# Kernel optimization log

Measured on AMD Instinct MI355X. Metric: run time of the kernel, lower is better.

The kernel has to match this reference:

```python
import jax, jax.numpy as jnp
import numpy as np

T = 64      # simulation_length
B = 128     # batch
D = 2048    # flattened input dim / axons per core
N = 2048    # neurons per core
L = 4       # number of cores (chain, latency = index)
OUT = 1024  # number of output_sources


def setup_inputs() -> dict:
    key = jax.random.key(0)
    k0, k1, k2, k3 = jax.random.split(key, 4)
    x = jax.random.uniform(k0, (B, D), dtype=jnp.float32)          # rate-coded input in [0,1)
    # core_params[l] = core_matrix.transpose() -> shape [N, A]; scaled for sane membrane dynamics
    W = jax.random.normal(k1, (L, N, D), dtype=jnp.float32) * 0.05
    thresholds = jnp.ones((L,), dtype=jnp.float32)
    # axon_sources: per-core irregular gather indices into previous core's neurons (input for l=0)
    axon_idx = jax.random.randint(k2, (L, D), 0, D, dtype=jnp.int32)
    out_idx = jax.random.randint(k3, (OUT,), 0, N, dtype=jnp.int32)
    return dict(x=x, W=W, thresholds=thresholds, axon_idx=axon_idx,
                out_idx=out_idx, simulation_length=T)


def _ideal_spike_scan(avg, thr, T):
    """Per-cycle: m += avg; spike = (m > thr); m[m > thr] -= thr.  avg: [B, N]."""
    def step(m, _):
        m = m + avg
        s = (m > thr).astype(m.dtype)
        return m - thr * s, s
    _, spikes = jax.lax.scan(step, jnp.zeros_like(avg), None, length=T)
    return spikes  # [T, B, N]


def reference(x, W, thresholds, axon_idx, out_idx, simulation_length):
    T = simulation_length
    L = W.shape[0]
    # generate_input_spike_train: x replicated across all cycles -> cache[-1]
    prev = jnp.broadcast_to(x, (T,) + x.shape)  # [T, B, D]
    for l in range(L):
        # get_signal_tensor: gather axon source signals for every cycle
        gathered = prev[:, :, axon_idx[l]]                    # [T, B, A]
        # per-cycle matmul: torch.matmul(core_params, sig.T).T == sig @ W[l].T
        val = jnp.einsum('tba,na->tbn', gathered, W[l])       # [T, B, N]
        avg = val.mean(axis=0)                                # avg_values [B, N]
        # ideal membrane integrate + threshold-reset recurrence -> out spike train
        prev = _ideal_spike_scan(avg, thresholds[l], T)       # [T, B, N]
    # output_signals: sum of output-source spikes over all cycles
    return prev[:, :, out_idx].sum(axis=0)                    # [B, OUT]
```

## Files before the change

### kernel.cpp

```cpp
#include <hip/hip_runtime.h>

#define BB   128
#define DD   2048
#define NN   2048
#define LL   4
#define OUTN 1024
#define JBQ  32
#define NDIG 5

#define NWDIG 12288
#define NG0   1024
#define NCSR  4

typedef double double4v __attribute__((ext_vector_type(4)));
typedef int    int4v    __attribute__((ext_vector_type(4)));
typedef char   char4v   __attribute__((ext_vector_type(4)));

__global__ __launch_bounds__(256) void prep_kernel(
    const float* __restrict__ W1,
    const float* __restrict__ x,
    const int*   __restrict__ axon,
    const int*   __restrict__ oidx,
    signed char* __restrict__ Wd,
    float*       __restrict__ At,
    int*         __restrict__ off,
    int*         __restrict__ lst)
{
    __shared__ int hist[2048];
    __shared__ int part[256];

    const int t  = threadIdx.x;
    const int bk = blockIdx.x;
    const size_t DP = (size_t)NN * DD;

    if (bk < NWDIG) {
        size_t i  = (size_t)bk * 256 + t;
        int    l  = (int)(i / (DP / 4));
        size_t e4 = i - (size_t)l * (DP / 4);
        int n = (int)(e4 >> 9);
        int k = (int)(e4 & 511) * 4;
        float4 w = *(const float4*)(W1 + (size_t)l * DP + (size_t)n * DD + k);
        const float wv[4] = {w.x, w.y, w.z, w.w};
        unsigned long long V[4];
        #pragma unroll
        for (int e = 0; e < 4; ++e)
            V[e] = (unsigned long long)(__double2ll_rn((double)wv[e] * 0x1p33)
                                        + (1LL << 34));
        signed char* base = Wd + (size_t)l * 5 * DP
                          + (size_t)(n >> 5) * 65536 + (size_t)(k >> 6) * 2048
                          + (n & 31) * 64 + (k & 63);
        #pragma unroll
        for (int j = 0; j < NDIG; ++j) {
            char4v p = { (char)((V[0] >> (7 * j)) & 127),
                         (char)((V[1] >> (7 * j)) & 127),
                         (char)((V[2] >> (7 * j)) & 127),
                         (char)((V[3] >> (7 * j)) & 127) };
            *(char4v*)(base + (size_t)j * DP) = p;
        }
        return;
    }
    if (bk < NWDIG + NG0) {
        int i = (bk - NWDIG) * 256 + t;
        int k = i >> 7;
        int b = i & 127;
        At[i] = x[b * DD + axon[k]];
        return;
    }
    {
        const int m   = bk - (NWDIG + NG0);
        const int* ip = (m < 3) ? (axon + (size_t)(m + 1) * DD) : oidx;
        const int cnt = (m < 3) ? DD : OUTN;
        int* offG = off + m * 2052;
        int* lstG = lst + m * 2048;

        for (int i = t; i < 2048; i += 256) hist[i] = 0;
        __syncthreads();
        for (int e = t; e < cnt; e += 256) atomicAdd(&hist[ip[e]], 1);
        __syncthreads();

        const int b0 = t * 8;
        int s = 0;
        #pragma unroll
        for (int i = 0; i < 8; ++i) s += hist[b0 + i];
        part[t] = s;
        __syncthreads();
        for (int d = 1; d < 256; d <<= 1) {
            int v = (t >= d) ? part[t - d] : 0;
            __syncthreads();
            part[t] += v;
            __syncthreads();
        }
        int base = part[t] - s;
        #pragma unroll
        for (int i = 0; i < 8; ++i) {
            int h = hist[b0 + i];
            offG[b0 + i] = base;
            hist[b0 + i] = base;
            base += h;
        }
        if (t == 255) offG[2048] = base;
        __syncthreads();
        for (int e = t; e < cnt; e += 256) {
            int n = ip[e];
            int pos = atomicAdd(&hist[n], 1);
            lstG[pos] = e;
        }
    }
}

__global__ __launch_bounds__(256, 2) void layer_kernel(
    const float* __restrict__ src,
    const int*   __restrict__ idx,
    int sR, int sB,
    const float* __restrict__ Wl,
    const float* __restrict__ thresholds, int l,
    const int*   __restrict__ Tptr,
    float* __restrict__ dst,
    const int* __restrict__ goff, const int* __restrict__ glst,
    signed char* __restrict__ g8n,
    const int* __restrict__ ooff, const int* __restrict__ olst,
    float* __restrict__ outp,
    int isLast)
{
    __shared__ double red[4 * 64 * 8];

    const int t    = threadIdx.x;
    const int wq   = t >> 6;
    const int lane = t & 63;
    const int q    = lane >> 4;
    const int c    = lane & 15;

    const int g     = blockIdx.x;
    const int btile = (g >> 3) & 7;
    const int nsup  = (g & 7) | ((g >> 6) << 3);
    const int n0    = nsup * 32;
    const int bcol  = btile * 16 + c;
    const size_t bo = (size_t)bcol * sB;

    double4v pr = {0., 0., 0., 0.}, pcv = {0., 0., 0., 0.};
    pr  = __builtin_amdgcn_mfma_f64_16x16x4f64(0.25 * (double)c, 1.0, pr, 0, 0, 0);
    pcv = __builtin_amdgcn_mfma_f64_16x16x4f64(0.25, (double)c, pcv, 0, 0, 0);
    int rowD[4], colD[4];
    #pragma unroll
    for (int r = 0; r < 4; ++r) {
        rowD[r] = (int)(pr[r] + 0.25);
        colD[r] = (int)(pcv[r] + 0.25);
    }

    double4v acc0[4] = {{0.,0.,0.,0.},{0.,0.,0.,0.},{0.,0.,0.,0.},{0.,0.,0.,0.}};
    double4v acc1[4] = {{0.,0.,0.,0.},{0.,0.,0.,0.},{0.,0.,0.,0.},{0.,0.,0.,0.}};

    const int    kbase = wq * (DD / 4);
    const float* wb0   = Wl + (size_t)(n0 + c) * DD + kbase + 4 * q;
    const float* wb1   = wb0 + (size_t)16 * DD;
    const int*   ibase = idx ? (idx + kbase + 4 * q) : nullptr;

    float4 wv0[4], wv1[4];
    float4 sv[4];
    int4   iv[4];

    #pragma unroll
    for (int p = 0; p < 4; ++p) {
        wv0[p] = *(const float4*)(wb0 + 16 * p);
        wv1[p] = *(const float4*)(wb1 + 16 * p);
    }
    #pragma unroll
    for (int p = 0; p < 4; ++p) {
        int r0, r1, r2, r3;
        if (ibase) {
            int4 iv0 = *(const int4*)(ibase + 16 * p);
            r0 = iv0.x; r1 = iv0.y; r2 = iv0.z; r3 = iv0.w;
        } else {
            int kb = kbase + 16 * p + 4 * q;
            r0 = kb; r1 = kb + 1; r2 = kb + 2; r3 = kb + 3;
        }
        sv[p].x = src[(size_t)r0 * sR + bo];
        sv[p].y = src[(size_t)r1 * sR + bo];
        sv[p].z = src[(size_t)r2 * sR + bo];
        sv[p].w = src[(size_t)r3 * sR + bo];
    }
    if (ibase) {
        #pragma unroll
        for (int p = 0; p < 4; ++p) iv[p] = *(const int4*)(ibase + 16 * (4 + p));
    }

    for (int u = 0; u < JBQ / 4; ++u) {
        #pragma unroll
        for (int gg = 0; gg < 4; ++gg) {
            float4 w0 = wv0[gg];
            float4 w1 = wv1[gg];
            float4 s  = sv[gg];

            int jn = 4 * u + 4 + gg; if (jn > JBQ - 1) jn = JBQ - 1;
            wv0[gg] = *(const float4*)(wb0 + 16 * jn);
            wv1[gg] = *(const float4*)(wb1 + 16 * jn);

            int r0, r1, r2, r3;
            if (ibase) {
                int4 ivv = iv[gg];
                r0 = ivv.x; r1 = ivv.y; r2 = ivv.z; r3 = ivv.w;
            } else {
                int kb = kbase + 16 * jn + 4 * q;
                r0 = kb; r1 = kb + 1; r2 = kb + 2; r3 = kb + 3;
            }
            sv[gg].x = src[(size_t)r0 * sR + bo];
            sv[gg].y = src[(size_t)r1 * sR + bo];
            sv[gg].z = src[(size_t)r2 * sR + bo];
            sv[gg].w = src[(size_t)r3 * sR + bo];

            if (ibase) {
                int jm = 4 * u + 8 + gg; if (jm > JBQ - 1) jm = JBQ - 1;
                iv[gg] = *(const int4*)(ibase + 16 * jm);
            }

            acc0[0] = __builtin_amdgcn_mfma_f64_16x16x4f64((double)w0.x, (double)s.x, acc0[0], 0, 0, 0);
            acc1[0] = __builtin_amdgcn_mfma_f64_16x16x4f64((double)w1.x, (double)s.x, acc1[0], 0, 0, 0);
            acc0[1] = __builtin_amdgcn_mfma_f64_16x16x4f64((double)w0.y, (double)s.y, acc0[1], 0, 0, 0);
            acc1[1] = __builtin_amdgcn_mfma_f64_16x16x4f64((double)w1.y, (double)s.y, acc1[1], 0, 0, 0);
            acc0[2] = __builtin_amdgcn_mfma_f64_16x16x4f64((double)w0.z, (double)s.z, acc0[2], 0, 0, 0);
            acc1[2] = __builtin_amdgcn_mfma_f64_16x16x4f64((double)w1.z, (double)s.z, acc1[2], 0, 0, 0);
            acc0[3] = __builtin_amdgcn_mfma_f64_16x16x4f64((double)w0.w, (double)s.w, acc0[3], 0, 0, 0);
            acc1[3] = __builtin_amdgcn_mfma_f64_16x16x4f64((double)w1.w, (double)s.w, acc1[3], 0, 0, 0);
        }
    }

    double4v a0 = (acc0[0] + acc0[1]) + (acc0[2] + acc0[3]);
    double4v a1 = (acc1[0] + acc1[1]) + (acc1[2] + acc1[3]);

    {
        double* my = red + ((size_t)wq * 64 + lane) * 8;
        #pragma unroll
        for (int r = 0; r < 4; ++r) { my[r] = a0[r]; my[4 + r] = a1[r]; }
    }
    __syncthreads();
    if (wq < 2) {
        const int off = wq * 4;
        double a[4];
        #pragma unroll
        for (int r = 0; r < 4; ++r) {
            a[r] =  red[((size_t)0 * 64 + lane) * 8 + off + r];
            a[r] += red[((size_t)1 * 64 + lane) * 8 + off + r];
            a[r] += red[((size_t)2 * 64 + lane) * 8 + off + r];
            a[r] += red[((size_t)3 * 64 + lane) * 8 + off + r];
        }

        const double th = (double)thresholds[l];
        const int T = *Tptr;
        const float sc = isLast ? 1.0f : (1.0f / (float)T);
        double m0 = 0., m1 = 0., m2 = 0., m3 = 0.;
        int c0 = 0, c1 = 0, c2 = 0, c3 = 0;
        for (int tt = 0; tt < T; ++tt) {
            m0 += a[0]; if (m0 > th) { c0++; m0 -= th; }
            m1 += a[1]; if (m1 > th) { c1++; m1 -= th; }
            m2 += a[2]; if (m2 > th) { c2++; m2 -= th; }
            m3 += a[3]; if (m3 > th) { c3++; m3 -= th; }
        }
        int cnt[4] = {c0, c1, c2, c3};
        #pragma unroll
        for (int r = 0; r < 4; ++r) {
            int n = n0 + 16 * wq + rowD[r];
            int b = btile * 16 + colD[r];
            if (dst)  dst[(size_t)n * BB + b] = (float)cnt[r] * sc;
            if (goff) {
                for (int j = goff[n]; j < goff[n + 1]; ++j) {
                    int k = glst[j];
                    g8n[(size_t)(k >> 6) * 8192 + b * 64 + (k & 63)] =
                        (signed char)cnt[r];
                }
            }
            if (ooff) {
                for (int j = ooff[n]; j < ooff[n + 1]; ++j)
                    outp[(size_t)b * OUTN + olst[j]] = (float)cnt[r];
            }
        }
    }
}

__global__ __launch_bounds__(256, 2) void layer_i8_kernel(
    const signed char* __restrict__ B8,
    const signed char* __restrict__ Wd5,
    const float* __restrict__ thresholds, int l,
    const int*   __restrict__ Tptr,
    const int* __restrict__ goff, const int* __restrict__ glst,
    signed char* __restrict__ g8n,
    const int* __restrict__ ooff, const int* __restrict__ olst,
    float* __restrict__ outp,
    int isLast)
{
    __shared__ double red[4 * 64 * 8];

    const int t    = threadIdx.x;
    const int wq   = t >> 6;
    const int lane = t & 63;
    const int q    = lane >> 4;
    const int c    = lane & 15;

    const int g     = blockIdx.x;
    const int btile = (g >> 3) & 7;
    const int nsup  = (g & 7) | ((g >> 6) << 3);
    const int n0    = nsup * 32;
    const int bcol  = btile * 16 + c;

    int rowD[4], colD[4];
    {
        const int cb  = c * 0x01010101;
        const int hot = (q == 0) ? 1 : 0;
        int4v aLab = {cb, cb, cb, cb};
        int4v oneh = {hot, 0, 0, 0};
        int4v dR = {0, 0, 0, 0}, dC = {0, 0, 0, 0};
        dR = __builtin_amdgcn_mfma_i32_16x16x64_i8(aLab, oneh, dR, 0, 0, 0);
        dC = __builtin_amdgcn_mfma_i32_16x16x64_i8(oneh, aLab, dC, 0, 0, 0);
        #pragma unroll
        for (int r = 0; r < 4; ++r) { rowD[r] = dR[r]; colD[r] = dC[r]; }
    }

    int4v acc0[NDIG], acc1[NDIG], accS = (int4v)0;
    #pragma unroll
    for (int j = 0; j < NDIG; ++j) { acc0[j] = (int4v)0; acc1[j] = (int4v)0; }

    const size_t DP = (size_t)NN * DD;
    const signed char* ab = Wd5 + (size_t)nsup * 65536 + c * 64 + q * 16;
    const signed char* bb = B8 + bcol * 64 + q * 16;

    const int4v ones = {0x01010101, 0x01010101, 0x01010101, 0x01010101};
    const int ck0 = wq * 8;

    int4v A0[NDIG], A1[NDIG], Bv;
    int4v N0[NDIG], N1[NDIG], Nb;

    {
        const signed char* ap = ab + (size_t)ck0 * 2048;
        #pragma unroll
        for (int j = 0; j < NDIG; ++j) {
            A0[j] = *(const int4v*)(ap + (size_t)j * DP);
            A1[j] = *(const int4v*)(ap + (size_t)j * DP + 1024);
        }
        Bv = *(const int4v*)(bb + (size_t)ck0 * 8192);
    }

    #pragma unroll 1
    for (int u = 0; u < 3; ++u) {
        {
            const signed char* ap = ab + (size_t)(ck0 + 2 * u + 1) * 2048;
            #pragma unroll
            for (int j = 0; j < NDIG; ++j) {
                N0[j] = *(const int4v*)(ap + (size_t)j * DP);
                N1[j] = *(const int4v*)(ap + (size_t)j * DP + 1024);
            }
            Nb = *(const int4v*)(bb + (size_t)(ck0 + 2 * u + 1) * 8192);
        }
        #pragma unroll
        for (int j = 0; j < NDIG; ++j) {
            acc0[j] = __builtin_amdgcn_mfma_i32_16x16x64_i8(A0[j], Bv, acc0[j], 0, 0, 0);
            acc1[j] = __builtin_amdgcn_mfma_i32_16x16x64_i8(A1[j], Bv, acc1[j], 0, 0, 0);
        }
        accS = __builtin_amdgcn_mfma_i32_16x16x64_i8(ones, Bv, accS, 0, 0, 0);
        {
            const signed char* ap = ab + (size_t)(ck0 + 2 * u + 2) * 2048;
            #pragma unroll
            for (int j = 0; j < NDIG; ++j) {
                A0[j] = *(const int4v*)(ap + (size_t)j * DP);
                A1[j] = *(const int4v*)(ap + (size_t)j * DP + 1024);
            }
            Bv = *(const int4v*)(bb + (size_t)(ck0 + 2 * u + 2) * 8192);
        }
        #pragma unroll
        for (int j = 0; j < NDIG; ++j) {
            acc0[j] = __builtin_amdgcn_mfma_i32_16x16x64_i8(N0[j], Nb, acc0[j], 0, 0, 0);
            acc1[j] = __builtin_amdgcn_mfma_i32_16x16x64_i8(N1[j], Nb, acc1[j], 0, 0, 0);
        }
        accS = __builtin_amdgcn_mfma_i32_16x16x64_i8(ones, Nb, accS, 0, 0, 0);
    }
    {
        const signed char* ap = ab + (size_t)(ck0 + 7) * 2048;
        #pragma unroll
        for (int j = 0; j < NDIG; ++j) {
            N0[j] = *(const int4v*)(ap + (size_t)j * DP);
            N1[j] = *(const int4v*)(ap + (size_t)j * DP + 1024);
        }
        Nb = *(const int4v*)(bb + (size_t)(ck0 + 7) * 8192);
    }
    #pragma unroll
    for (int j = 0; j < NDIG; ++j) {
        acc0[j] = __builtin_amdgcn_mfma_i32_16x16x64_i8(A0[j], Bv, acc0[j], 0, 0, 0);
        acc1[j] = __builtin_amdgcn_mfma_i32_16x16x64_i8(A1[j], Bv, acc1[j], 0, 0, 0);
    }
    accS = __builtin_amdgcn_mfma_i32_16x16x64_i8(ones, Bv, accS, 0, 0, 0);
    #pragma unroll
    for (int j = 0; j < NDIG; ++j) {
        acc0[j] = __builtin_amdgcn_mfma_i32_16x16x64_i8(N0[j], Nb, acc0[j], 0, 0, 0);
        acc1[j] = __builtin_amdgcn_mfma_i32_16x16x64_i8(N1[j], Nb, acc1[j], 0, 0, 0);
    }
    accS = __builtin_amdgcn_mfma_i32_16x16x64_i8(ones, Nb, accS, 0, 0, 0);

    const double S0 = 0x1p-33, S1 = 0x1p-26, S2 = 0x1p-19,
                 S3 = 0x1p-12, S4 = 0x1p-5;
    {
        double* my = red + ((size_t)wq * 64 + lane) * 8;
        #pragma unroll
        for (int r = 0; r < 4; ++r) {
            double corr = 2.0 * (double)accS[r];
            my[r]     = S0 * (double)acc0[0][r] + S1 * (double)acc0[1][r]
                      + S2 * (double)acc0[2][r] + S3 * (double)acc0[3][r]
                      + S4 * (double)acc0[4][r] - corr;
            my[4 + r] = S0 * (double)acc1[0][r] + S1 * (double)acc1[1][r]
                      + S2 * (double)acc1[2][r] + S3 * (double)acc1[3][r]
                      + S4 * (double)acc1[4][r] - corr;
        }
    }
    __syncthreads();
    if (wq < 2) {
        const int off = wq * 4;
        double a[4];
        #pragma unroll
        for (int r = 0; r < 4; ++r) {
            a[r] =  red[((size_t)0 * 64 + lane) * 8 + off + r];
            a[r] += red[((size_t)1 * 64 + lane) * 8 + off + r];
            a[r] += red[((size_t)2 * 64 + lane) * 8 + off + r];
            a[r] += red[((size_t)3 * 64 + lane) * 8 + off + r];
        }

        const double th = (double)thresholds[l];
        const int T = *Tptr;
        const double invT = 1.0 / (double)T;
        double m0 = 0., m1 = 0., m2 = 0., m3 = 0.;
        int c0 = 0, c1 = 0, c2 = 0, c3 = 0;
        const double v0 = a[0] * invT, v1 = a[1] * invT,
                     v2 = a[2] * invT, v3 = a[3] * invT;
        for (int tt = 0; tt < T; ++tt) {
            m0 += v0; if (m0 > th) { c0++; m0 -= th; }
            m1 += v1; if (m1 > th) { c1++; m1 -= th; }
            m2 += v2; if (m2 > th) { c2++; m2 -= th; }
            m3 += v3; if (m3 > th) { c3++; m3 -= th; }
        }
        int cnt[4] = {c0, c1, c2, c3};
        #pragma unroll
        for (int r = 0; r < 4; ++r) {
            int n = n0 + 16 * wq + rowD[r];
            int b = btile * 16 + colD[r];
            if (goff) {
                for (int j = goff[n]; j < goff[n + 1]; ++j) {
                    int k = glst[j];
                    g8n[(size_t)(k >> 6) * 8192 + b * 64 + (k & 63)] =
                        (signed char)cnt[r];
                }
            }
            if (ooff) {
                for (int j = ooff[n]; j < ooff[n + 1]; ++j)
                    outp[(size_t)b * OUTN + olst[j]] = (float)cnt[r];
            }
        }
    }
}

__global__ __launch_bounds__(256) void out_kernel(
    const float* __restrict__ cntT, const int* __restrict__ out_idx,
    float* __restrict__ out)
{
    int i = blockIdx.x * 256 + threadIdx.x;
    int b = i >> 10;
    int o = i & 1023;
    out[i] = cntT[(size_t)out_idx[o] * BB + b];
}

extern "C" void kernel_launch(void* const* d_in, const int* in_sizes, int n_in,
                              void* d_out, int out_size, void* d_ws, size_t ws_size,
                              hipStream_t stream)
{
    const float* x    = (const float*)d_in[0];
    const float* W    = (const float*)d_in[1];
    const float* thr  = (const float*)d_in[2];
    const int*   axon = (const int*)d_in[3];
    const int*   oidx = (const int*)d_in[4];
    const int*   Tptr = (const int*)d_in[5];
    float* out = (float*)d_out;

    const size_t DP = (size_t)NN * DD;
    char* ws = (char*)d_ws;
    float* At   = (float*)ws;
    float* mA   = (float*)(ws + (1u << 20));
    float* mB   = (float*)(ws + (2u << 20));
    float* cntT = (float*)(ws + (3u << 20));
    signed char* g8A = (signed char*)(ws + (4u << 20));
    signed char* g8B = (signed char*)(ws + (4u << 20) + (256u << 10));
    int* off = (int*)(ws + (4u << 20) + (512u << 10));
    int* lst = (int*)(ws + (4u << 20) + (640u << 10));
    signed char* Wd  = (signed char*)(ws + (5u << 20));

    const int useI8 = (ws_size >= ((size_t)80 << 20)) ? 1 : 0;

    if (!useI8) {
        const float* srcs[LL] = { x, mA, mB, mA };
        float*       dsts[LL] = { mA, mB, mA, cntT };
        for (int l = 0; l < LL; ++l) {
            layer_kernel<<<512, 256, 0, stream>>>(
                srcs[l], axon + (size_t)l * DD,
                (l == 0) ? 1 : BB, (l == 0) ? DD : 1,
                W + (size_t)l * NN * DD, thr, l, Tptr,
                dsts[l], nullptr, nullptr, nullptr, nullptr, nullptr, nullptr,
                (l == LL - 1) ? 1 : 0);
        }
        out_kernel<<<(BB * OUTN) / 256, 256, 0, stream>>>(cntT, oidx, out);
        return;
    }

    prep_kernel<<<NWDIG + NG0 + NCSR, 256, 0, stream>>>(
        W + DP, x, axon, oidx, Wd, At, off, lst);

    layer_kernel<<<512, 256, 0, stream>>>(
        At, nullptr, BB, 1, W, thr, 0, Tptr,
        nullptr, off + 0 * 2052, lst + 0 * 2048, g8A,
        nullptr, nullptr, nullptr, 0);

    layer_i8_kernel<<<512, 256, 0, stream>>>(
        g8A, Wd + 0 * 5 * DP, thr, 1, Tptr,
        off + 1 * 2052, lst + 1 * 2048, g8B,
        nullptr, nullptr, nullptr, 0);
    layer_i8_kernel<<<512, 256, 0, stream>>>(
        g8B, Wd + 1 * 5 * DP, thr, 2, Tptr,
        off + 2 * 2052, lst + 2 * 2048, g8A,
        nullptr, nullptr, nullptr, 0);
    layer_i8_kernel<<<512, 256, 0, stream>>>(
        g8A, Wd + 2 * 5 * DP, thr, 3, Tptr,
        nullptr, nullptr, nullptr,
        off + 3 * 2052, lst + 3 * 2048, out, 1);
}
```

Baseline: 215.1 us.

## Fuse prep and all layer kernels into one persistent kernel with grid barriers

Replaces the five separate launches (prep, fp64 layer 0, three int8 layers) with a single 512-block persistent kernel. Grid-wide atomic-counter barriers separate the stages, and the barrier counters are zeroed with a memset before launch. The aim is to remove launch gaps and tail effects between stages. In exchange, each block now does 24× more weight-digit preparation work serially. Correctness depends on all 512 blocks being co-resident, which the launch bounds allowing two blocks per CU are meant to ensure.

```diff
diff --git a/kernel.cpp b/kernel.cpp
--- a/kernel.cpp
+++ b/kernel.cpp
@@ -7,39 +7,220 @@
 #define OUTN 1024
 #define JBQ  32
 #define NDIG 5
-
-#define NWDIG 12288
-#define NG0   1024
-#define NCSR  4
+#define GRID 512
 
 typedef double double4v __attribute__((ext_vector_type(4)));
 typedef int    int4v    __attribute__((ext_vector_type(4)));
 typedef char   char4v   __attribute__((ext_vector_type(4)));
 
-__global__ __launch_bounds__(256) void prep_kernel(
-    const float* __restrict__ W1,
-    const float* __restrict__ x,
-    const int*   __restrict__ axon,
-    const int*   __restrict__ oidx,
-    signed char* __restrict__ Wd,
-    float*       __restrict__ At,
-    int*         __restrict__ off,
-    int*         __restrict__ lst)
+__device__ __forceinline__ void bar_sync(int* bar, int idx)
 {
-    __shared__ int hist[2048];
-    __shared__ int part[256];
-
-    const int t  = threadIdx.x;
-    const int bk = blockIdx.x;
+    __syncthreads();
+    if (threadIdx.x == 0) {
+        __threadfence();
+        atomicAdd(&bar[idx], 1);
+        while (atomicAdd(&bar[idx], 0) < GRID)
+            __builtin_amdgcn_s_sleep(4);
+        __threadfence();
+    }
+    __syncthreads();
+}
+
+__device__ __forceinline__ void i8_layer_body(
+    const signed char* __restrict__ B8,
+    const signed char* __restrict__ Wd5,
+    const float* __restrict__ thresholds, int l, int T,
+    const int* __restrict__ goff, const int* __restrict__ glst,
+    signed char* __restrict__ g8n,
+    const int* __restrict__ ooff, const int* __restrict__ olst,
+    float* __restrict__ outp,
+    double* red)
+{
+    const int t    = threadIdx.x;
+    const int wq   = t >> 6;
+    const int lane = t & 63;
+    const int q    = lane >> 4;
+    const int c    = lane & 15;
+
+    const int g     = blockIdx.x;
+    const int btile = (g >> 3) & 7;
+    const int nsup  = (g & 7) | ((g >> 6) << 3);
+    const int n0    = nsup * 32;
+    const int bcol  = btile * 16 + c;
+
+    int rowD[4], colD[4];
+    {
+        const int cb  = c * 0x01010101;
+        const int hot = (q == 0) ? 1 : 0;
+        int4v aLab = {cb, cb, cb, cb};
+        int4v oneh = {hot, 0, 0, 0};
+        int4v dR = {0, 0, 0, 0}, dC = {0, 0, 0, 0};
+        dR = __builtin_amdgcn_mfma_i32_16x16x64_i8(aLab, oneh, dR, 0, 0, 0);
+        dC = __builtin_amdgcn_mfma_i32_16x16x64_i8(oneh, aLab, dC, 0, 0, 0);
+        #pragma unroll
+        for (int r = 0; r < 4; ++r) { rowD[r] = dR[r]; colD[r] = dC[r]; }
+    }
+
+    int4v acc0[NDIG], acc1[NDIG], accS = (int4v)0;
+    #pragma unroll
+    for (int j = 0; j < NDIG; ++j) { acc0[j] = (int4v)0; acc1[j] = (int4v)0; }
+
     const size_t DP = (size_t)NN * DD;
-
-    if (bk < NWDIG) {
-        size_t i  = (size_t)bk * 256 + t;
+    const signed char* ab = Wd5 + (size_t)nsup * 65536 + c * 64 + q * 16;
+    const signed char* bb = B8 + bcol * 64 + q * 16;
+
+    const int4v ones = {0x01010101, 0x01010101, 0x01010101, 0x01010101};
+    const int ck0 = wq * 8;
+
+    int4v A0[NDIG], A1[NDIG], Bv;
+    int4v N0[NDIG], N1[NDIG], Nb;
+
+    {
+        const signed char* ap = ab + (size_t)ck0 * 2048;
+        #pragma unroll
+        for (int j = 0; j < NDIG; ++j) {
+            A0[j] = *(const int4v*)(ap + (size_t)j * DP);
+            A1[j] = *(const int4v*)(ap + (size_t)j * DP + 1024);
+        }
+        Bv = *(const int4v*)(bb + (size_t)ck0 * 8192);
+    }
+
+    #pragma unroll 1
+    for (int u = 0; u < 3; ++u) {
+        {
+            const signed char* ap = ab + (size_t)(ck0 + 2 * u + 1) * 2048;
+            #pragma unroll
+            for (int j = 0; j < NDIG; ++j) {
+                N0[j] = *(const int4v*)(ap + (size_t)j * DP);
+                N1[j] = *(const int4v*)(ap + (size_t)j * DP + 1024);
+            }
+            Nb = *(const int4v*)(bb + (size_t)(ck0 + 2 * u + 1) * 8192);
+        }
+        #pragma unroll
+        for (int j = 0; j < NDIG; ++j) {
+            acc0[j] = __builtin_amdgcn_mfma_i32_16x16x64_i8(A0[j], Bv, acc0[j], 0, 0, 0);
+            acc1[j] = __builtin_amdgcn_mfma_i32_16x16x64_i8(A1[j], Bv, acc1[j], 0, 0, 0);
+        }
+        accS = __builtin_amdgcn_mfma_i32_16x16x64_i8(ones, Bv, accS, 0, 0, 0);
+        {
+            const signed char* ap = ab + (size_t)(ck0 + 2 * u + 2) * 2048;
+            #pragma unroll
+            for (int j = 0; j < NDIG; ++j) {
+                A0[j] = *(const int4v*)(ap + (size_t)j * DP);
+                A1[j] = *(const int4v*)(ap + (size_t)j * DP + 1024);
+            }
+            Bv = *(const int4v*)(bb + (size_t)(ck0 + 2 * u + 2) * 8192);
+        }
+        #pragma unroll
+        for (int j = 0; j < NDIG; ++j) {
+            acc0[j] = __builtin_amdgcn_mfma_i32_16x16x64_i8(N0[j], Nb, acc0[j], 0, 0, 0);
+            acc1[j] = __builtin_amdgcn_mfma_i32_16x16x64_i8(N1[j], Nb, acc1[j], 0, 0, 0);
+        }
+        accS = __builtin_amdgcn_mfma_i32_16x16x64_i8(ones, Nb, accS, 0, 0, 0);
+    }
+    {
+        const signed char* ap = ab + (size_t)(ck0 + 7) * 2048;
+        #pragma unroll
+        for (int j = 0; j < NDIG; ++j) {
+            N0[j] = *(const int4v*)(ap + (size_t)j * DP);
+            N1[j] = *(const int4v*)(ap + (size_t)j * DP + 1024);
+        }
+        Nb = *(const int4v*)(bb + (size_t)(ck0 + 7) * 8192);
+    }
+    #pragma unroll
+    for (int j = 0; j < NDIG; ++j) {
+        acc0[j] = __builtin_amdgcn_mfma_i32_16x16x64_i8(A0[j], Bv, acc0[j], 0, 0, 0);
+        acc1[j] = __builtin_amdgcn_mfma_i32_16x16x64_i8(A1[j], Bv, acc1[j], 0, 0, 0);
+    }
+    accS = __builtin_amdgcn_mfma_i32_16x16x64_i8(ones, Bv, accS, 0, 0, 0);
+    #pragma unroll
+    for (int j = 0; j < NDIG; ++j) {
+        acc0[j] = __builtin_amdgcn_mfma_i32_16x16x64_i8(N0[j], Nb, acc0[j], 0, 0, 0);
+        acc1[j] = __builtin_amdgcn_mfma_i32_16x16x64_i8(N1[j], Nb, acc1[j], 0, 0, 0);
+    }
+    accS = __builtin_amdgcn_mfma_i32_16x16x64_i8(ones, Nb, accS, 0, 0, 0);
+
+    const double S0 = 0x1p-33, S1 = 0x1p-26, S2 = 0x1p-19,
+                 S3 = 0x1p-12, S4 = 0x1p-5;
+    {
+        double* my = red + ((size_t)wq * 64 + lane) * 8;
+        #pragma unroll
+        for (int r = 0; r < 4; ++r) {
+            double corr = 2.0 * (double)accS[r];
+            my[r]     = S0 * (double)acc0[0][r] + S1 * (double)acc0[1][r]
+                      + S2 * (double)acc0[2][r] + S3 * (double)acc0[3][r]
+                      + S4 * (double)acc0[4][r] - corr;
+            my[4 + r] = S0 * (double)acc1[0][r] + S1 * (double)acc1[1][r]
+                      + S2 * (double)acc1[2][r] + S3 * (double)acc1[3][r]
+                      + S4 * (double)acc1[4][r] - corr;
+        }
+    }
+    __syncthreads();
+    if (wq < 2) {
+        const int off = wq * 4;
+        double a[4];
+        #pragma unroll
+        for (int r = 0; r < 4; ++r) {
+            a[r] =  red[((size_t)0 * 64 + lane) * 8 + off + r];
+            a[r] += red[((size_t)1 * 64 + lane) * 8 + off + r];
+            a[r] += red[((size_t)2 * 64 + lane) * 8 + off + r];
+            a[r] += red[((size_t)3 * 64 + lane) * 8 + off + r];
+        }
+
+        const double th = (double)thresholds[l];
+        const double invT = 1.0 / (double)T;
+        double m0 = 0., m1 = 0., m2 = 0., m3 = 0.;
+        int c0 = 0, c1 = 0, c2 = 0, c3 = 0;
+        const double v0 = a[0] * invT, v1 = a[1] * invT,
+                     v2 = a[2] * invT, v3 = a[3] * invT;
+        for (int tt = 0; tt < T; ++tt) {
+            m0 += v0; if (m0 > th) { c0++; m0 -= th; }
+            m1 += v1; if (m1 > th) { c1++; m1 -= th; }
+            m2 += v2; if (m2 > th) { c2++; m2 -= th; }
+            m3 += v3; if (m3 > th) { c3++; m3 -= th; }
+        }
+        int cnt[4] = {c0, c1, c2, c3};
+        #pragma unroll
+        for (int r = 0; r < 4; ++r) {
+            int n = n0 + 16 * wq + rowD[r];
+            int b = btile * 16 + colD[r];
+            if (goff) {
+                for (int j = goff[n]; j < goff[n + 1]; ++j) {
+                    int k = glst[j];
+                    g8n[(size_t)(k >> 6) * 8192 + b * 64 + (k & 63)] =
+                        (signed char)cnt[r];
+                }
+            }
+            if (ooff) {
+                for (int j = ooff[n]; j < ooff[n + 1]; ++j)
+                    outp[(size_t)b * OUTN + olst[j]] = (float)cnt[r];
+            }
+        }
+    }
+}
+
+__global__ __launch_bounds__(256, 2) void mega_kernel(
+    const float* __restrict__ x, const float* __restrict__ W,
+    const float* __restrict__ thr, const int* __restrict__ axon,
+    const int* __restrict__ oidx, const int* __restrict__ Tptr,
+    float* __restrict__ out,
+    signed char* __restrict__ Wd, float* __restrict__ At,
+    signed char* __restrict__ g8A, signed char* __restrict__ g8B,
+    int* __restrict__ off, int* __restrict__ lst, int* __restrict__ bar)
+{
+    __shared__ double red[4 * 64 * 8];
+
+    const int t = threadIdx.x;
+    const int g = blockIdx.x;
+    const size_t DP = (size_t)NN * DD;
+
+    for (int u = 0; u < 24; ++u) {
+        size_t i  = (size_t)(g * 24 + u) * 256 + t;
         int    l  = (int)(i / (DP / 4));
         size_t e4 = i - (size_t)l * (DP / 4);
         int n = (int)(e4 >> 9);
         int k = (int)(e4 & 511) * 4;
-        float4 w = *(const float4*)(W1 + (size_t)l * DP + (size_t)n * DD + k);
+        float4 w = *(const float4*)(W + DP + (size_t)l * DP + (size_t)n * DD + k);
         const float wv[4] = {w.x, w.y, w.z, w.w};
         unsigned long long V[4];
         #pragma unroll
@@ -57,17 +238,17 @@
                          (char)((V[3] >> (7 * j)) & 127) };
             *(char4v*)(base + (size_t)j * DP) = p;
         }
-        return;
-    }
-    if (bk < NWDIG + NG0) {
-        int i = (bk - NWDIG) * 256 + t;
+    }
+    for (int u = 0; u < 2; ++u) {
+        int i = (g * 2 + u) * 256 + t;
         int k = i >> 7;
         int b = i & 127;
         At[i] = x[b * DD + axon[k]];
-        return;
-    }
-    {
-        const int m   = bk - (NWDIG + NG0);
+    }
+    if (g < 4) {
+        int* hist = (int*)red;
+        int* part = ((int*)red) + 2048;
+        const int m   = g;
         const int* ip = (m < 3) ? (axon + (size_t)(m + 1) * DD) : oidx;
         const int cnt = (m < 3) ? DD : OUTN;
         int* offG = off + m * 2052;
@@ -106,6 +287,139 @@
             lstG[pos] = e;
         }
     }
+    bar_sync(bar, 0);
+
+    {
+        const int wq   = t >> 6;
+        const int lane = t & 63;
+        const int q    = lane >> 4;
+        const int c    = lane & 15;
+        const int btile = (g >> 3) & 7;
+        const int nsup  = (g & 7) | ((g >> 6) << 3);
+        const int n0    = nsup * 32;
+        const int bcol  = btile * 16 + c;
+
+        double4v pr = {0., 0., 0., 0.}, pcv = {0., 0., 0., 0.};
+        pr  = __builtin_amdgcn_mfma_f64_16x16x4f64(0.25 * (double)c, 1.0, pr, 0, 0, 0);
+        pcv = __builtin_amdgcn_mfma_f64_16x16x4f64(0.25, (double)c, pcv, 0, 0, 0);
+        int rowD[4], colD[4];
+        #pragma unroll
+        for (int r = 0; r < 4; ++r) {
+            rowD[r] = (int)(pr[r] + 0.25);
+            colD[r] = (int)(pcv[r] + 0.25);
+        }
+
+        double4v acc0[4] = {{0.,0.,0.,0.},{0.,0.,0.,0.},{0.,0.,0.,0.},{0.,0.,0.,0.}};
+        double4v acc1[4] = {{0.,0.,0.,0.},{0.,0.,0.,0.},{0.,0.,0.,0.},{0.,0.,0.,0.}};
+
+        const int    kbase = wq * (DD / 4);
+        const float* wb0   = W + (size_t)(n0 + c) * DD + kbase + 4 * q;
+        const float* wb1   = wb0 + (size_t)16 * DD;
+
+        float4 wv0[4], wv1[4];
+        float4 sv[4];
+
+        #pragma unroll
+        for (int p = 0; p < 4; ++p) {
+            wv0[p] = *(const float4*)(wb0 + 16 * p);
+            wv1[p] = *(const float4*)(wb1 + 16 * p);
+        }
+        #pragma unroll
+        for (int p = 0; p < 4; ++p) {
+            int kb = kbase + 16 * p + 4 * q;
+            sv[p].x = At[(size_t)(kb + 0) * BB + bcol];
+            sv[p].y = At[(size_t)(kb + 1) * BB + bcol];
+            sv[p].z = At[(size_t)(kb + 2) * BB + bcol];
+            sv[p].w = At[(size_t)(kb + 3) * BB + bcol];
+        }
+
+        for (int u = 0; u < JBQ / 4; ++u) {
+            #pragma unroll
+            for (int gg = 0; gg < 4; ++gg) {
+                float4 w0 = wv0[gg];
+                float4 w1 = wv1[gg];
+                float4 s  = sv[gg];
+
+                int jn = 4 * u + 4 + gg; if (jn > JBQ - 1) jn = JBQ - 1;
+                wv0[gg] = *(const float4*)(wb0 + 16 * jn);
+                wv1[gg] = *(const float4*)(wb1 + 16 * jn);
+
+                int kb = kbase + 16 * jn + 4 * q;
+                sv[gg].x = At[(size_t)(kb + 0) * BB + bcol];
+                sv[gg].y = At[(size_t)(kb + 1) * BB + bcol];
+                sv[gg].z = At[(size_t)(kb + 2) * BB + bcol];
+                sv[gg].w = At[(size_t)(kb + 3) * BB + bcol];
+
+                acc0[0] = __builtin_amdgcn_mfma_f64_16x16x4f64((double)w0.x, (double)s.x, acc0[0], 0, 0, 0);
+                acc1[0] = __builtin_amdgcn_mfma_f64_16x16x4f64((double)w1.x, (double)s.x, acc1[0], 0, 0, 0);
+                acc0[1] = __builtin_amdgcn_mfma_f64_16x16x4f64((double)w0.y, (double)s.y, acc0[1], 0, 0, 0);
+                acc1[1] = __builtin_amdgcn_mfma_f64_16x16x4f64((double)w1.y, (double)s.y, acc1[1], 0, 0, 0);
+                acc0[2] = __builtin_amdgcn_mfma_f64_16x16x4f64((double)w0.z, (double)s.z, acc0[2], 0, 0, 0);
+                acc1[2] = __builtin_amdgcn_mfma_f64_16x16x4f64((double)w1.z, (double)s.z, acc1[2], 0, 0, 0);
+                acc0[3] = __builtin_amdgcn_mfma_f64_16x16x4f64((double)w0.w, (double)s.w, acc0[3], 0, 0, 0);
+                acc1[3] = __builtin_amdgcn_mfma_f64_16x16x4f64((double)w1.w, (double)s.w, acc1[3], 0, 0, 0);
+            }
+        }
+
+        double4v a0 = (acc0[0] + acc0[1]) + (acc0[2] + acc0[3]);
+        double4v a1 = (acc1[0] + acc1[1]) + (acc1[2] + acc1[3]);
+
+        {
+            double* my = red + ((size_t)wq * 64 + lane) * 8;
+            #pragma unroll
+            for (int r = 0; r < 4; ++r) { my[r] = a0[r]; my[4 + r] = a1[r]; }
+        }
+        __syncthreads();
+        if (wq < 2) {
+            const int off4 = wq * 4;
+            double a[4];
+            #pragma unroll
+            for (int r = 0; r < 4; ++r) {
+                a[r] =  red[((size_t)0 * 64 + lane) * 8 + off4 + r];
+                a[r] += red[((size_t)1 * 64 + lane) * 8 + off4 + r];
+                a[r] += red[((size_t)2 * 64 + lane) * 8 + off4 + r];
+                a[r] += red[((size_t)3 * 64 + lane) * 8 + off4 + r];
+            }
+
+            const double th = (double)thr[0];
+            const int T = *Tptr;
+            double m0 = 0., m1 = 0., m2 = 0., m3 = 0.;
+            int c0 = 0, c1 = 0, c2 = 0, c3 = 0;
+            for (int tt = 0; tt < T; ++tt) {
+                m0 += a[0]; if (m0 > th) { c0++; m0 -= th; }
+                m1 += a[1]; if (m1 > th) { c1++; m1 -= th; }
+                m2 += a[2]; if (m2 > th) { c2++; m2 -= th; }
+                m3 += a[3]; if (m3 > th) { c3++; m3 -= th; }
+            }
+            int cnt[4] = {c0, c1, c2, c3};
+            const int* goff = off + 0 * 2052;
+            const int* glst = lst + 0 * 2048;
+            #pragma unroll
+            for (int r = 0; r < 4; ++r) {
+                int n = n0 + 16 * wq + rowD[r];
+                int b = btile * 16 + colD[r];
+                for (int j = goff[n]; j < goff[n + 1]; ++j) {
+                    int k = glst[j];
+                    g8A[(size_t)(k >> 6) * 8192 + b * 64 + (k & 63)] =
+                        (signed char)cnt[r];
+                }
+            }
+        }
+    }
+    bar_sync(bar, 1);
+
+    const int T = *Tptr;
+    i8_layer_body(g8A, Wd + 0 * 5 * DP, thr, 1, T,
+                  off + 1 * 2052, lst + 1 * 2048, g8B,
+                  nullptr, nullptr, nullptr, red);
+    bar_sync(bar, 2);
+    i8_layer_body(g8B, Wd + 1 * 5 * DP, thr, 2, T,
+                  off + 2 * 2052, lst + 2 * 2048, g8A,
+                  nullptr, nullptr, nullptr, red);
+    bar_sync(bar, 3);
+    i8_layer_body(g8A, Wd + 2 * 5 * DP, thr, 3, T,
+                  nullptr, nullptr, nullptr,
+                  off + 3 * 2052, lst + 3 * 2048, out, red);
 }
 
 __global__ __launch_bounds__(256, 2) void layer_kernel(
@@ -115,12 +429,7 @@
     const float* __restrict__ Wl,
     const float* __restrict__ thresholds, int l,
     const int*   __restrict__ Tptr,
-    float* __restrict__ dst,
-    const int* __restrict__ goff, const int* __restrict__ glst,
-    signed char* __restrict__ g8n,
-    const int* __restrict__ ooff, const int* __restrict__ olst,
-    float* __restrict__ outp,
-    int isLast)
+    float* __restrict__ dst, int isLast)
 {
     __shared__ double red[4 * 64 * 8];
 
@@ -260,195 +569,7 @@
         for (int r = 0; r < 4; ++r) {
             int n = n0 + 16 * wq + rowD[r];
             int b = btile * 16 + colD[r];
-            if (dst)  dst[(size_t)n * BB + b] = (float)cnt[r] * sc;
-            if (goff) {
-                for (int j = goff[n]; j < goff[n + 1]; ++j) {
-                    int k = glst[j];
-                    g8n[(size_t)(k >> 6) * 8192 + b * 64 + (k & 63)] =
-                        (signed char)cnt[r];
-                }
-            }
-            if (ooff) {
-                for (int j = ooff[n]; j < ooff[n + 1]; ++j)
-                    outp[(size_t)b * OUTN + olst[j]] = (float)cnt[r];
-            }
-        }
-    }
-}
-
-__global__ __launch_bounds__(256, 2) void layer_i8_kernel(
-    const signed char* __restrict__ B8,
-    const signed char* __restrict__ Wd5,
-    const float* __restrict__ thresholds, int l,
-    const int*   __restrict__ Tptr,
-    const int* __restrict__ goff, const int* __restrict__ glst,
-    signed char* __restrict__ g8n,
-    const int* __restrict__ ooff, const int* __restrict__ olst,
-    float* __restrict__ outp,
-    int isLast)
-{
-    __shared__ double red[4 * 64 * 8];
-
-    const int t    = threadIdx.x;
-    const int wq   = t >> 6;
-    const int lane = t & 63;
-    const int q    = lane >> 4;
-    const int c    = lane & 15;
-
-    const int g     = blockIdx.x;
-    const int btile = (g >> 3) & 7;
-    const int nsup  = (g & 7) | ((g >> 6) << 3);
-    const int n0    = nsup * 32;
-    const int bcol  = btile * 16 + c;
-
-    int rowD[4], colD[4];
-    {
-        const int cb  = c * 0x01010101;
-        const int hot = (q == 0) ? 1 : 0;
-        int4v aLab = {cb, cb, cb, cb};
-        int4v oneh = {hot, 0, 0, 0};
-        int4v dR = {0, 0, 0, 0}, dC = {0, 0, 0, 0};
-        dR = __builtin_amdgcn_mfma_i32_16x16x64_i8(aLab, oneh, dR, 0, 0, 0);
-        dC = __builtin_amdgcn_mfma_i32_16x16x64_i8(oneh, aLab, dC, 0, 0, 0);
-        #pragma unroll
-        for (int r = 0; r < 4; ++r) { rowD[r] = dR[r]; colD[r] = dC[r]; }
-    }
-
-    int4v acc0[NDIG], acc1[NDIG], accS = (int4v)0;
-    #pragma unroll
-    for (int j = 0; j < NDIG; ++j) { acc0[j] = (int4v)0; acc1[j] = (int4v)0; }
-
-    const size_t DP = (size_t)NN * DD;
-    const signed char* ab = Wd5 + (size_t)nsup * 65536 + c * 64 + q * 16;
-    const signed char* bb = B8 + bcol * 64 + q * 16;
-
-    const int4v ones = {0x01010101, 0x01010101, 0x01010101, 0x01010101};
-    const int ck0 = wq * 8;
-
-    int4v A0[NDIG], A1[NDIG], Bv;
-    int4v N0[NDIG], N1[NDIG], Nb;
-
-    {
-        const signed char* ap = ab + (size_t)ck0 * 2048;
-        #pragma unroll
-        for (int j = 0; j < NDIG; ++j) {
-            A0[j] = *(const int4v*)(ap + (size_t)j * DP);
-            A1[j] = *(const int4v*)(ap + (size_t)j * DP + 1024);
-        }
-        Bv = *(const int4v*)(bb + (size_t)ck0 * 8192);
-    }
-
-    #pragma unroll 1
-    for (int u = 0; u < 3; ++u) {
-        {
-            const signed char* ap = ab + (size_t)(ck0 + 2 * u + 1) * 2048;
-            #pragma unroll
-            for (int j = 0; j < NDIG; ++j) {
-                N0[j] = *(const int4v*)(ap + (size_t)j * DP);
-                N1[j] = *(const int4v*)(ap + (size_t)j * DP + 1024);
-            }
-            Nb = *(const int4v*)(bb + (size_t)(ck0 + 2 * u + 1) * 8192);
-        }
-        #pragma unroll
-        for (int j = 0; j < NDIG; ++j) {
-            acc0[j] = __builtin_amdgcn_mfma_i32_16x16x64_i8(A0[j], Bv, acc0[j], 0, 0, 0);
-            acc1[j] = __builtin_amdgcn_mfma_i32_16x16x64_i8(A1[j], Bv, acc1[j], 0, 0, 0);
-        }
-        accS = __builtin_amdgcn_mfma_i32_16x16x64_i8(ones, Bv, accS, 0, 0, 0);
-        {
-            const signed char* ap = ab + (size_t)(ck0 + 2 * u + 2) * 2048;
-            #pragma unroll
-            for (int j = 0; j < NDIG; ++j) {
-                A0[j] = *(const int4v*)(ap + (size_t)j * DP);
-                A1[j] = *(const int4v*)(ap + (size_t)j * DP + 1024);
-            }
-            Bv = *(const int4v*)(bb + (size_t)(ck0 + 2 * u + 2) * 8192);
-        }
-        #pragma unroll
-        for (int j = 0; j < NDIG; ++j) {
-            acc0[j] = __builtin_amdgcn_mfma_i32_16x16x64_i8(N0[j], Nb, acc0[j], 0, 0, 0);
-            acc1[j] = __builtin_amdgcn_mfma_i32_16x16x64_i8(N1[j], Nb, acc1[j], 0, 0, 0);
-        }
-        accS = __builtin_amdgcn_mfma_i32_16x16x64_i8(ones, Nb, accS, 0, 0, 0);
-    }
-    {
-        const signed char* ap = ab + (size_t)(ck0 + 7) * 2048;
-        #pragma unroll
-        for (int j = 0; j < NDIG; ++j) {
-            N0[j] = *(const int4v*)(ap + (size_t)j * DP);
-            N1[j] = *(const int4v*)(ap + (size_t)j * DP + 1024);
-        }
-        Nb = *(const int4v*)(bb + (size_t)(ck0 + 7) * 8192);
-    }
-    #pragma unroll
-    for (int j = 0; j < NDIG; ++j) {
-        acc0[j] = __builtin_amdgcn_mfma_i32_16x16x64_i8(A0[j], Bv, acc0[j], 0, 0, 0);
-        acc1[j] = __builtin_amdgcn_mfma_i32_16x16x64_i8(A1[j], Bv, acc1[j], 0, 0, 0);
-    }
-    accS = __builtin_amdgcn_mfma_i32_16x16x64_i8(ones, Bv, accS, 0, 0, 0);
-    #pragma unroll
-    for (int j = 0; j < NDIG; ++j) {
-        acc0[j] = __builtin_amdgcn_mfma_i32_16x16x64_i8(N0[j], Nb, acc0[j], 0, 0, 0);
-        acc1[j] = __builtin_amdgcn_mfma_i32_16x16x64_i8(N1[j], Nb, acc1[j], 0, 0, 0);
-    }
-    accS = __builtin_amdgcn_mfma_i32_16x16x64_i8(ones, Nb, accS, 0, 0, 0);
-
-    const double S0 = 0x1p-33, S1 = 0x1p-26, S2 = 0x1p-19,
-                 S3 = 0x1p-12, S4 = 0x1p-5;
-    {
-        double* my = red + ((size_t)wq * 64 + lane) * 8;
-        #pragma unroll
-        for (int r = 0; r < 4; ++r) {
-            double corr = 2.0 * (double)accS[r];
-            my[r]     = S0 * (double)acc0[0][r] + S1 * (double)acc0[1][r]
-                      + S2 * (double)acc0[2][r] + S3 * (double)acc0[3][r]
-                      + S4 * (double)acc0[4][r] - corr;
-            my[4 + r] = S0 * (double)acc1[0][r] + S1 * (double)acc1[1][r]
-                      + S2 * (double)acc1[2][r] + S3 * (double)acc1[3][r]
-                      + S4 * (double)acc1[4][r] - corr;
-        }
-    }
-    __syncthreads();
-    if (wq < 2) {
-        const int off = wq * 4;
-        double a[4];
-        #pragma unroll
-        for (int r = 0; r < 4; ++r) {
-            a[r] =  red[((size_t)0 * 64 + lane) * 8 + off + r];
-            a[r] += red[((size_t)1 * 64 + lane) * 8 + off + r];
-            a[r] += red[((size_t)2 * 64 + lane) * 8 + off + r];
-            a[r] += red[((size_t)3 * 64 + lane) * 8 + off + r];
-        }
-
-        const double th = (double)thresholds[l];
-        const int T = *Tptr;
-        const double invT = 1.0 / (double)T;
-        double m0 = 0., m1 = 0., m2 = 0., m3 = 0.;
-        int c0 = 0, c1 = 0, c2 = 0, c3 = 0;
-        const double v0 = a[0] * invT, v1 = a[1] * invT,
-                     v2 = a[2] * invT, v3 = a[3] * invT;
-        for (int tt = 0; tt < T; ++tt) {
-            m0 += v0; if (m0 > th) { c0++; m0 -= th; }
-            m1 += v1; if (m1 > th) { c1++; m1 -= th; }
-            m2 += v2; if (m2 > th) { c2++; m2 -= th; }
-            m3 += v3; if (m3 > th) { c3++; m3 -= th; }
-        }
-        int cnt[4] = {c0, c1, c2, c3};
-        #pragma unroll
-        for (int r = 0; r < 4; ++r) {
-            int n = n0 + 16 * wq + rowD[r];
-            int b = btile * 16 + colD[r];
-            if (goff) {
-                for (int j = goff[n]; j < goff[n + 1]; ++j) {
-                    int k = glst[j];
-                    g8n[(size_t)(k >> 6) * 8192 + b * 64 + (k & 63)] =
-                        (signed char)cnt[r];
-                }
-            }
-            if (ooff) {
-                for (int j = ooff[n]; j < ooff[n + 1]; ++j)
-                    outp[(size_t)b * OUTN + olst[j]] = (float)cnt[r];
-            }
+            dst[(size_t)n * BB + b] = (float)cnt[r] * sc;
         }
     }
 }
@@ -475,7 +596,6 @@
     const int*   Tptr = (const int*)d_in[5];
     float* out = (float*)d_out;
 
-    const size_t DP = (size_t)NN * DD;
     char* ws = (char*)d_ws;
     float* At   = (float*)ws;
     float* mA   = (float*)(ws + (1u << 20));
@@ -485,6 +605,7 @@
     signed char* g8B = (signed char*)(ws + (4u << 20) + (256u << 10));
     int* off = (int*)(ws + (4u << 20) + (512u << 10));
     int* lst = (int*)(ws + (4u << 20) + (640u << 10));
+    int* bar = (int*)(ws + (4u << 20) + (768u << 10));
     signed char* Wd  = (signed char*)(ws + (5u << 20));
 
     const int useI8 = (ws_size >= ((size_t)80 << 20)) ? 1 : 0;
@@ -497,31 +618,13 @@
                 srcs[l], axon + (size_t)l * DD,
                 (l == 0) ? 1 : BB, (l == 0) ? DD : 1,
                 W + (size_t)l * NN * DD, thr, l, Tptr,
-                dsts[l], nullptr, nullptr, nullptr, nullptr, nullptr, nullptr,
-                (l == LL - 1) ? 1 : 0);
+                dsts[l], (l == LL - 1) ? 1 : 0);
         }
         out_kernel<<<(BB * OUTN) / 256, 256, 0, stream>>>(cntT, oidx, out);
         return;
     }
 
-    prep_kernel<<<NWDIG + NG0 + NCSR, 256, 0, stream>>>(
-        W + DP, x, axon, oidx, Wd, At, off, lst);
-
-    layer_kernel<<<512, 256, 0, stream>>>(
-        At, nullptr, BB, 1, W, thr, 0, Tptr,
-        nullptr, off + 0 * 2052, lst + 0 * 2048, g8A,
-        nullptr, nullptr, nullptr, 0);
-
-    layer_i8_kernel<<<512, 256, 0, stream>>>(
-        g8A, Wd + 0 * 5 * DP, thr, 1, Tptr,
-        off + 1 * 2052, lst + 1 * 2048, g8B,
-        nullptr, nullptr, nullptr, 0);
-    layer_i8_kernel<<<512, 256, 0, stream>>>(
-        g8B, Wd + 1 * 5 * DP, thr, 2, Tptr,
-        off + 2 * 2052, lst + 2 * 2048, g8A,
-        nullptr, nullptr, nullptr, 0);
-    layer_i8_kernel<<<512, 256, 0, stream>>>(
-        g8A, Wd + 2 * 5 * DP, thr, 3, Tptr,
-        nullptr, nullptr, nullptr,
-        off + 3 * 2052, lst + 3 * 2048, out, 1);
+    hipMemsetAsync(bar, 0, 64, stream);
+    mega_kernel<<<GRID, 256, 0, stream>>>(
+        x, W, thr, axon, oidx, Tptr, out, Wd, At, g8A, g8B, off, lst, bar);
 }
```

Measured after the change: 454.2 us. 2.11x slower.
